# Kernel tuning notes

Measured on AMD Instinct MI355X. Metric: run time of the kernel, lower is better.

Reference implementation:

```python
import jax, jax.numpy as jnp
import numpy as np

D_MODEL = 1024
D_FF = 4096
NUM_EXPERTS = 8
TOP_K = 2
SEQ = 1024
BATCH = 2


def setup_inputs() -> dict:
    key = jax.random.key(0)
    ks = jax.random.split(key, 7)
    s = 0.02
    x = jax.random.normal(ks[0], (SEQ, BATCH, D_MODEL), dtype=jnp.float32)
    gate_w = jax.random.normal(ks[1], (D_MODEL, NUM_EXPERTS), dtype=jnp.float32) * s
    gate_b = jnp.zeros((NUM_EXPERTS,), dtype=jnp.float32)
    W1 = jax.random.normal(ks[2], (NUM_EXPERTS, D_MODEL, D_FF), dtype=jnp.float32) * s
    b1 = jnp.zeros((NUM_EXPERTS, D_FF), dtype=jnp.float32)
    W2 = jax.random.normal(ks[3], (NUM_EXPERTS, D_FF, D_MODEL), dtype=jnp.float32) * s
    b2 = jnp.zeros((NUM_EXPERTS, D_MODEL), dtype=jnp.float32)
    return {"x": x, "gate_w": gate_w, "gate_b": gate_b,
            "W1": W1, "b1": b1, "W2": W2, "b2": b2}


def reference(x, gate_w, gate_b, W1, b1, W2, b2):
    S, B, D = x.shape
    x_flat = x.reshape(-1, D)                       # [T, D], T = S*B
    scores = x_flat @ gate_w + gate_b               # [T, E]
    topk_vals, topk_idx = jax.lax.top_k(scores, TOP_K)   # [T, K]
    topk_probs = jax.nn.softmax(topk_vals, axis=-1)      # [T, K]
    # combine weight per (token, expert): sum of probs over slots routed to e
    one_hot = jax.nn.one_hot(topk_idx, NUM_EXPERTS, dtype=x.dtype)  # [T, K, E]
    combine = jnp.einsum('tk,tke->te', topk_probs, one_hot)         # [T, E]
    # dense per-expert FFN (tokens with combine weight 0 contribute nothing,
    # matching the masked gather/scatter in the torch loop)
    h = jax.nn.relu(jnp.einsum('td,edf->etf', x_flat, W1) + b1[:, None, :])  # [E, T, F]
    y = jnp.einsum('etf,efd->etd', h, W2) + b2[:, None, :]                    # [E, T, D]
    out = jnp.einsum('te,etd->td', combine, y)       # [T, D]
    return out.reshape(S, B, D)
```

## Files before the change

### kernel.cpp

```cpp
#include <hip/hip_runtime.h>
#include <stdint.h>

#define T_TOKENS 2048
#define DM 1024
#define DF 4096
#define NEXP 8
#define NSLOTS (T_TOKENS * 2)

typedef __bf16 bf16x8 __attribute__((ext_vector_type(8)));
typedef float f32x4 __attribute__((ext_vector_type(4)));

__device__ __forceinline__ ushort f2bf(float f) {
    union { float f; uint32_t u; } v; v.f = f;
    uint32_t r = v.u + 0x7FFFu + ((v.u >> 16) & 1u);
    return (ushort)(r >> 16);
}

__device__ __forceinline__ void gload16(const ushort* g, ushort* l) {
    __builtin_amdgcn_global_load_lds(
        (const __attribute__((address_space(1))) uint32_t*)g,
        (__attribute__((address_space(3))) uint32_t*)l,
        16, 0, 0);
}

__global__ void init_cnt(uint32_t* cnt) {
    if (threadIdx.x < NEXP) cnt[threadIdx.x] = 0;
}

__global__ __launch_bounds__(256) void gate_route(
    const float* __restrict__ x, const float* __restrict__ gw,
    const float* __restrict__ gb,
    uint32_t* __restrict__ route, uint32_t* __restrict__ cnt,
    float* __restrict__ prob)
{
    const int w = threadIdx.x >> 6;
    const int lane = threadIdx.x & 63;
    const int t = blockIdx.x * 4 + w;
    float acc[NEXP];
#pragma unroll
    for (int e = 0; e < NEXP; ++e) acc[e] = 0.f;
    const float* xr = x + (size_t)t * DM;
#pragma unroll
    for (int j = 0; j < DM / 64; ++j) {
        const int d = j * 64 + lane;
        const float xv = xr[d];
        const float* g = gw + (size_t)d * NEXP;
#pragma unroll
        for (int e = 0; e < NEXP; ++e) acc[e] += xv * g[e];
    }
#pragma unroll
    for (int e = 0; e < NEXP; ++e) {
#pragma unroll
        for (int off = 32; off > 0; off >>= 1)
            acc[e] += __shfl_xor(acc[e], off);
        acc[e] += gb[e];
    }
    if (lane == 0) {
        int e0 = 0; float v0 = acc[0];
#pragma unroll
        for (int e = 1; e < NEXP; ++e) if (acc[e] > v0) { v0 = acc[e]; e0 = e; }
        int e1 = -1; float v1 = -1e30f;
#pragma unroll
        for (int e = 0; e < NEXP; ++e) if (e != e0 && acc[e] > v1) { v1 = acc[e]; e1 = e; }
        const float ex = expf(v1 - v0);
        const float inv = 1.f / (1.f + ex);
        prob[t * 2 + 0] = inv;
        prob[t * 2 + 1] = ex * inv;
        uint32_t pos = atomicAdd(&cnt[e0], 1u);
        route[e0 * T_TOKENS + pos] = (uint32_t)(t * 2);
        pos = atomicAdd(&cnt[e1], 1u);
        route[e1 * T_TOKENS + pos] = (uint32_t)(t * 2 + 1);
    }
}

__global__ __launch_bounds__(256) void convert_x(const float* __restrict__ x,
                                                 ushort* __restrict__ xb)
{
    const int i = (blockIdx.x * 256 + threadIdx.x) * 4;
    const float4 v = *reinterpret_cast<const float4*>(x + i);
    ushort4 o;
    o.x = f2bf(v.x); o.y = f2bf(v.y); o.z = f2bf(v.z); o.w = f2bf(v.w);
    *reinterpret_cast<ushort4*>(xb + i) = o;
}

template<int K, int N>
__global__ __launch_bounds__(256) void conv_transpose(const float* __restrict__ W,
                                                      ushort* __restrict__ Wb)
{
    const int e  = blockIdx.y;
    const int nt = blockIdx.x % (N / 64);
    const int kt = blockIdx.x / (N / 64);
    const int k0 = kt * 64, n0 = nt * 64;
    __shared__ ushort T[64][80];
    const int t = threadIdx.x;
    const int kr = t >> 4, nc = (t & 15) * 4;
    const float* src = W + ((size_t)e * K + k0 + kr) * N + n0 + nc;
#pragma unroll
    for (int i = 0; i < 4; ++i) {
        const float4 v = *reinterpret_cast<const float4*>(src + (size_t)i * 16 * N);
        T[nc + 0][kr + i * 16] = f2bf(v.x);
        T[nc + 1][kr + i * 16] = f2bf(v.y);
        T[nc + 2][kr + i * 16] = f2bf(v.z);
        T[nc + 3][kr + i * 16] = f2bf(v.w);
    }
    __syncthreads();
    const int r = t >> 2, c0 = t & 3;
    ushort* dst = Wb + ((size_t)e * N + n0 + r) * K + k0;
#pragma unroll
    for (int i = 0; i < 2; ++i) {
        const int c = c0 + i * 4;
        const uint4 v = *reinterpret_cast<const uint4*>(&T[r][c * 8]);
        *reinterpret_cast<uint4*>(dst + c * 8) = v;
    }
}

template<int KD, int ND, bool FIRST, int SPLIT, int NT>
__global__ __launch_bounds__(256, 4) void moe_gemm5(
    const ushort* __restrict__ Abuf,
    const ushort* __restrict__ Wb,
    const float* __restrict__ bias,
    const uint32_t* __restrict__ route,
    const uint32_t* __restrict__ cnt,
    const float* __restrict__ prob,
    ushort* __restrict__ hout,
    float* __restrict__ yout)
{
    const int bx = blockIdx.x;
    const int e  = bx / (16 * NT);
    const int mt = (bx / NT) & 15;
    const int nt = bx % NT;
    const uint32_t cntE = cnt[e];
    const int m0 = mt * 128;
    if ((uint32_t)m0 >= cntE) return;
    const int n0 = nt * 128;
    const int z  = (SPLIT > 1) ? (int)blockIdx.z : 0;
    const int kbeg = z * (KD / SPLIT);
    const int niter = (KD / SPLIT) / 32;

    __shared__ ushort As[2][128 * 32];
    __shared__ ushort Bs[2][128 * 32];
    __shared__ uint32_t s_route[128];

    const int tid = threadIdx.x;
    if (tid < 128) {
        const uint32_t idx = (uint32_t)(m0 + tid);
        s_route[tid] = (idx < cntE) ? route[e * T_TOKENS + idx] : 0xFFFFFFFFu;
    }
    __syncthreads();

    const int w = tid >> 6, l = tid & 63;

    const ushort* asrc[2];
    const ushort* bsrc[2];
#pragma unroll
    for (int i = 0; i < 2; ++i) {
        const int chunk = (w * 2 + i) * 64 + l;
        const int row = chunk >> 2;
        const int c   = chunk & 3;
        const int cs  = c ^ ((row >> 1) & 3);
        const uint32_t s = s_route[row];
        const size_t ar = (s == 0xFFFFFFFFu) ? 0 : (FIRST ? (size_t)(s >> 1) : (size_t)s);
        asrc[i] = Abuf + ar * KD + cs * 8 + kbeg;
        bsrc[i] = Wb + ((size_t)e * ND + n0 + row) * KD + cs * 8 + kbeg;
    }

    f32x4 acc[4][4];
#pragma unroll
    for (int i = 0; i < 4; ++i)
#pragma unroll
        for (int j = 0; j < 4; ++j) acc[i][j] = (f32x4){0.f, 0.f, 0.f, 0.f};

    const int q = l & 15, g = l >> 4;
    const int wm = w >> 1, wn = w & 1;

    int aoff[4], boff[4];
#pragma unroll
    for (int mi = 0; mi < 4; ++mi) {
        int row = wm * 64 + mi * 16 + q;
        aoff[mi] = row * 64 + (g ^ ((row >> 1) & 3)) * 16;
        row = wn * 64 + mi * 16 + q;
        boff[mi] = row * 64 + (g ^ ((row >> 1) & 3)) * 16;
    }

    ushort* const abase0 = &As[0][0];
    ushort* const bbase0 = &Bs[0][0];

#pragma unroll
    for (int i = 0; i < 2; ++i) gload16(asrc[i], abase0 + (w * 2 + i) * 512);
#pragma unroll
    for (int i = 0; i < 2; ++i) gload16(bsrc[i], bbase0 + (w * 2 + i) * 512);

    int cur = 0;
    for (int t = 0; t < niter; ++t) {
        if (t + 1 < niter) {
            ushort* ad = abase0 + (cur ^ 1) * (128 * 32) + (w * 2) * 512;
            ushort* bd = bbase0 + (cur ^ 1) * (128 * 32) + (w * 2) * 512;
            const int k1 = (t + 1) * 32;
#pragma unroll
            for (int i = 0; i < 2; ++i) gload16(asrc[i] + k1, ad + i * 512);
#pragma unroll
            for (int i = 0; i < 2; ++i) gload16(bsrc[i] + k1, bd + i * 512);
            asm volatile("s_waitcnt vmcnt(4)" ::: "memory");
        } else {
            asm volatile("s_waitcnt vmcnt(0)" ::: "memory");
        }
        __builtin_amdgcn_s_barrier();
        __builtin_amdgcn_sched_barrier(0);

        const char* Ab = (const char*)(abase0 + cur * (128 * 32));
        const char* Bb = (const char*)(bbase0 + cur * (128 * 32));
        bf16x8 af[4], bv[4];
#pragma unroll
        for (int mi = 0; mi < 4; ++mi)
            af[mi] = *reinterpret_cast<const bf16x8*>(Ab + aoff[mi]);
#pragma unroll
        for (int ni = 0; ni < 4; ++ni)
            bv[ni] = *reinterpret_cast<const bf16x8*>(Bb + boff[ni]);
        __builtin_amdgcn_s_setprio(1);
#pragma unroll
        for (int mi = 0; mi < 4; ++mi)
#pragma unroll
            for (int ni = 0; ni < 4; ++ni)
                acc[mi][ni] = __builtin_amdgcn_mfma_f32_16x16x32_bf16(
                    af[mi], bv[ni], acc[mi][ni], 0, 0, 0);
        __builtin_amdgcn_s_setprio(0);
        __builtin_amdgcn_s_barrier();
        cur ^= 1;
    }

    const float* brow = bias + (size_t)e * ND;
#pragma unroll
    for (int mi = 0; mi < 4; ++mi) {
#pragma unroll
        for (int ni = 0; ni < 4; ++ni) {
            const int gcol = n0 + wn * 64 + ni * 16 + q;
            const float bv = (SPLIT == 1 || z == 0) ? brow[gcol] : 0.f;
#pragma unroll
            for (int j = 0; j < 4; ++j) {
                const int row = wm * 64 + mi * 16 + g * 4 + j;
                if ((uint32_t)(m0 + row) < cntE) {
                    const uint32_t s = s_route[row];
                    float v = acc[mi][ni][j] + bv;
                    if (FIRST) {
                        v = fmaxf(v, 0.f);
                        hout[(size_t)s * ND + gcol] = f2bf(v);
                    } else {
                        yout[((size_t)z * NSLOTS + s) * ND + gcol] = v * prob[s];
                    }
                }
            }
        }
    }
}

__global__ __launch_bounds__(256) void combine4(const float* __restrict__ yc,
                                                float* __restrict__ out)
{
    const int gid = blockIdx.x * 256 + threadIdx.x;
    const int t = gid >> 8;
    const int dq = gid & 255;
    const float4* Y = reinterpret_cast<const float4*>(yc);
    float4 o = {0.f, 0.f, 0.f, 0.f};
#pragma unroll
    for (int zz = 0; zz < 4; ++zz) {
#pragma unroll
        for (int k = 0; k < 2; ++k) {
            const float4 v = Y[((size_t)zz * NSLOTS + 2 * t + k) * 256 + dq];
            o.x += v.x; o.y += v.y; o.z += v.z; o.w += v.w;
        }
    }
    reinterpret_cast<float4*>(out)[gid] = o;
}

template<int KD, int ND, bool FIRST>
__global__ __launch_bounds__(256) void moe_gemm_v1(
    const ushort* __restrict__ Abuf, const float* __restrict__ W,
    const float* __restrict__ bias, const uint32_t* __restrict__ route,
    const uint32_t* __restrict__ cnt, const float* __restrict__ prob,
    ushort* __restrict__ hout, float* __restrict__ yout)
{
    const int e = blockIdx.x >> 4;
    const int mt = blockIdx.x & 15;
    const uint32_t cntE = cnt[e];
    const int m0 = mt * 128;
    if ((uint32_t)m0 >= cntE) return;
    const int n0 = blockIdx.y * 128;
    const int tid = threadIdx.x;
    __shared__ ushort Asm[128][40];
    __shared__ ushort Bsm[128][40];
    __shared__ uint32_t s_route[128];
    if (tid < 128) {
        const uint32_t idx = (uint32_t)(m0 + tid);
        s_route[tid] = (idx < cntE) ? route[e * T_TOKENS + idx] : 0xFFFFFFFFu;
    }
    __syncthreads();
    const int ar = tid >> 1, ah = tid & 1;
    const uint32_t s_a = s_route[ar];
    size_t arow = 0;
    if (s_a != 0xFFFFFFFFu) arow = FIRST ? (size_t)(s_a >> 1) : (size_t)s_a;
    const ushort* asrc = Abuf + arow * KD + ah * 16;
    const int c4 = tid & 31, kq = tid >> 5;
    const float* wbase = W + (size_t)e * KD * ND + (size_t)n0 + (size_t)c4 * 4;
    f32x4 acc[4][4];
#pragma unroll
    for (int i = 0; i < 4; ++i)
#pragma unroll
        for (int j = 0; j < 4; ++j) acc[i][j] = (f32x4){0.f, 0.f, 0.f, 0.f};
    const int lane = tid & 63, wv = tid >> 6;
    const int wm = wv >> 1, wn = wv & 1;
    const int q = lane & 15, g = lane >> 4;
    for (int k0 = 0; k0 < KD; k0 += 32) {
        {
            const uint4* src = reinterpret_cast<const uint4*>(asrc + k0);
            const uint4 v0 = src[0];
            const uint4 v1 = src[1];
            *reinterpret_cast<uint4*>(&Asm[ar][ah * 16]) = v0;
            *reinterpret_cast<uint4*>(&Asm[ar][ah * 16 + 8]) = v1;
        }
        {
            ushort vals[4][4];
#pragma unroll
            for (int r = 0; r < 4; ++r) {
                const float4 v = *reinterpret_cast<const float4*>(
                    wbase + (size_t)(k0 + kq * 4 + r) * ND);
                vals[r][0] = f2bf(v.x); vals[r][1] = f2bf(v.y);
                vals[r][2] = f2bf(v.z); vals[r][3] = f2bf(v.w);
            }
#pragma unroll
            for (int c = 0; c < 4; ++c) {
                const ushort4 o = { vals[0][c], vals[1][c], vals[2][c], vals[3][c] };
                *reinterpret_cast<ushort4*>(&Bsm[c4 * 4 + c][kq * 4]) = o;
            }
        }
        __syncthreads();
        bf16x8 af[4], bfr[4];
#pragma unroll
        for (int mi = 0; mi < 4; ++mi)
            af[mi] = *reinterpret_cast<const bf16x8*>(&Asm[wm * 64 + mi * 16 + q][g * 8]);
#pragma unroll
        for (int ni = 0; ni < 4; ++ni)
            bfr[ni] = *reinterpret_cast<const bf16x8*>(&Bsm[wn * 64 + ni * 16 + q][g * 8]);
#pragma unroll
        for (int mi = 0; mi < 4; ++mi)
#pragma unroll
            for (int ni = 0; ni < 4; ++ni)
                acc[mi][ni] = __builtin_amdgcn_mfma_f32_16x16x32_bf16(
                    af[mi], bfr[ni], acc[mi][ni], 0, 0, 0);
        __syncthreads();
    }
#pragma unroll
    for (int mi = 0; mi < 4; ++mi) {
#pragma unroll
        for (int ni = 0; ni < 4; ++ni) {
            const int gcol = n0 + wn * 64 + ni * 16 + q;
#pragma unroll
            for (int j = 0; j < 4; ++j) {
                const int row = wm * 64 + mi * 16 + g * 4 + j;
                if ((uint32_t)(m0 + row) < cntE) {
                    const uint32_t s = s_route[row];
                    float v = acc[mi][ni][j] + bias[e * ND + gcol];
                    if (FIRST) {
                        v = fmaxf(v, 0.f);
                        hout[(size_t)s * ND + gcol] = f2bf(v);
                    } else {
                        yout[(size_t)s * ND + gcol] = v * prob[s];
                    }
                }
            }
        }
    }
}

__global__ __launch_bounds__(256) void combine1(const float* __restrict__ yc,
                                                float* __restrict__ out)
{
    const int gid = blockIdx.x * 256 + threadIdx.x;
    const int t = gid >> 8;
    const int dq = gid & 255;
    const float4 va = reinterpret_cast<const float4*>(yc)[(size_t)(2 * t) * 256 + dq];
    const float4 vb = reinterpret_cast<const float4*>(yc)[(size_t)(2 * t + 1) * 256 + dq];
    const float4 o = { va.x + vb.x, va.y + vb.y, va.z + vb.z, va.w + vb.w };
    reinterpret_cast<float4*>(out)[gid] = o;
}

extern "C" void kernel_launch(void* const* d_in, const int* in_sizes, int n_in,
                              void* d_out, int out_size, void* d_ws, size_t ws_size,
                              hipStream_t stream)
{
    const float* x  = (const float*)d_in[0];
    const float* gw = (const float*)d_in[1];
    const float* gb = (const float*)d_in[2];
    const float* W1 = (const float*)d_in[3];
    const float* b1 = (const float*)d_in[4];
    const float* W2 = (const float*)d_in[5];
    const float* b2 = (const float*)d_in[6];
    float* out = (float*)d_out;
    char* ws = (char*)d_ws;

    const size_t OFF_XB    = 0;
    const size_t OFF_H     = 4194304;
    const size_t OFF_ROUTE = 37748736;
    const size_t OFF_CNT   = 37814272;
    const size_t OFF_PROB  = 37814336;
    const size_t OFF_W1B   = 38797312;
    const size_t OFF_W2B   = 105906176;
    const size_t OFF_YC    = OFF_W1B;
    const size_t NEED      = 173015040ull;

    if (ws_size >= NEED) {
        ushort*   xb    = (ushort*)(ws + OFF_XB);
        ushort*   h     = (ushort*)(ws + OFF_H);
        float*    yc    = (float*)(ws + OFF_YC);
        uint32_t* route = (uint32_t*)(ws + OFF_ROUTE);
        uint32_t* cnt   = (uint32_t*)(ws + OFF_CNT);
        float*    prob  = (float*)(ws + OFF_PROB);
        ushort*   w1b   = (ushort*)(ws + OFF_W1B);
        ushort*   w2b   = (ushort*)(ws + OFF_W2B);

        hipLaunchKernelGGL(init_cnt, dim3(1), dim3(64), 0, stream, cnt);
        hipLaunchKernelGGL(gate_route, dim3(T_TOKENS / 4), dim3(256), 0, stream,
                           x, gw, gb, route, cnt, prob);
        hipLaunchKernelGGL(convert_x, dim3(T_TOKENS * DM / 1024), dim3(256), 0, stream, x, xb);
        hipLaunchKernelGGL((conv_transpose<DM, DF>), dim3((DM / 64) * (DF / 64), NEXP),
                           dim3(256), 0, stream, W1, w1b);
        hipLaunchKernelGGL((conv_transpose<DF, DM>), dim3((DF / 64) * (DM / 64), NEXP),
                           dim3(256), 0, stream, W2, w2b);
        hipLaunchKernelGGL((moe_gemm5<DM, DF, true, 1, 32>),
                           dim3(NEXP * 16 * 32, 1, 1), dim3(256), 0, stream,
                           xb, w1b, b1, route, cnt, prob, h, (float*)nullptr);
        hipLaunchKernelGGL((moe_gemm5<DF, DM, false, 4, 8>),
                           dim3(NEXP * 16 * 8, 1, 4), dim3(256), 0, stream,
                           h, w2b, b2, route, cnt, prob, (ushort*)nullptr, yc);
        hipLaunchKernelGGL(combine4, dim3(T_TOKENS * DM / 1024), dim3(256), 0, stream, yc, out);
    } else {
        const size_t F_XB = 0, F_H = 4194304, F_YC = 37748736;
        const size_t F_ROUTE = 54525952, F_CNT = 54591488, F_PROB = 54591552;
        ushort*   xb    = (ushort*)(ws + F_XB);
        ushort*   h     = (ushort*)(ws + F_H);
        float*    yc    = (float*)(ws + F_YC);
        uint32_t* route = (uint32_t*)(ws + F_ROUTE);
        uint32_t* cnt   = (uint32_t*)(ws + F_CNT);
        float*    prob  = (float*)(ws + F_PROB);

        hipLaunchKernelGGL(init_cnt, dim3(1), dim3(64), 0, stream, cnt);
        hipLaunchKernelGGL(gate_route, dim3(T_TOKENS / 4), dim3(256), 0, stream,
                           x, gw, gb, route, cnt, prob);
        hipLaunchKernelGGL(convert_x, dim3(T_TOKENS * DM / 1024), dim3(256), 0, stream, x, xb);
        hipLaunchKernelGGL((moe_gemm_v1<DM, DF, true>), dim3(NEXP * 16, DF / 128),
                           dim3(256), 0, stream, xb, W1, b1, route, cnt, prob,
                           h, (float*)nullptr);
        hipLaunchKernelGGL((moe_gemm_v1<DF, DM, false>), dim3(NEXP * 16, DM / 128),
                           dim3(256), 0, stream, h, W2, b2, route, cnt, prob,
                           (ushort*)nullptr, yc);
        hipLaunchKernelGGL(combine1, dim3(T_TOKENS * DM / 1024), dim3(256), 0, stream, yc, out);
    }
}
```

Baseline: 315.7 us.

## Store hidden activations expert-contiguous and fold gate probability into first GEMM

The first GEMM now writes the hidden activations into rows grouped contiguously by expert, using a prefix-sum offset table, and scales them by the routing probability there. The second GEMM then reads its A operand as contiguous rows with no route indirection. Bias and probability handling for the second GEMM move into the combine kernel, which locates each token's two slot rows through a new packed expert/position array. The W2 conversion is also reordered after the first GEMM. This removes gathered reads and the route lookup from the larger GEMM, at the cost of an extra tiny launch and scattered reads in combine.

Result: faster. 305.5 us (-3.2%).

```diff
diff --git a/kernel.cpp b/kernel.cpp
--- a/kernel.cpp
+++ b/kernel.cpp
@@ -6,6 +6,7 @@
 #define DF 4096
 #define NEXP 8
 #define NSLOTS (T_TOKENS * 2)
+#define HROWS (NSLOTS + 128)
 
 typedef __bf16 bf16x8 __attribute__((ext_vector_type(8)));
 typedef float f32x4 __attribute__((ext_vector_type(4)));
@@ -31,7 +32,7 @@
     const float* __restrict__ x, const float* __restrict__ gw,
     const float* __restrict__ gb,
     uint32_t* __restrict__ route, uint32_t* __restrict__ cnt,
-    float* __restrict__ prob)
+    float* __restrict__ prob, uint32_t* __restrict__ epk)
 {
     const int w = threadIdx.x >> 6;
     const int lane = threadIdx.x & 63;
@@ -68,8 +69,21 @@
         prob[t * 2 + 1] = ex * inv;
         uint32_t pos = atomicAdd(&cnt[e0], 1u);
         route[e0 * T_TOKENS + pos] = (uint32_t)(t * 2);
+        epk[t * 2] = ((uint32_t)e0 << 16) | pos;
         pos = atomicAdd(&cnt[e1], 1u);
         route[e1 * T_TOKENS + pos] = (uint32_t)(t * 2 + 1);
+        epk[t * 2 + 1] = ((uint32_t)e1 << 16) | pos;
+    }
+}
+
+__global__ void prefix_offs(const uint32_t* __restrict__ cnt,
+                            uint32_t* __restrict__ offs)
+{
+    if (threadIdx.x == 0) {
+        uint32_t a = 0;
+#pragma unroll
+        for (int e = 0; e < NEXP; ++e) { offs[e] = a; a += cnt[e]; }
+        offs[NEXP] = a;
     }
 }
 
@@ -115,12 +129,13 @@
 }
 
 template<int KD, int ND, bool FIRST, int SPLIT, int NT>
-__global__ __launch_bounds__(256, 4) void moe_gemm5(
+__global__ __launch_bounds__(256, 4) void moe_gemm6(
     const ushort* __restrict__ Abuf,
     const ushort* __restrict__ Wb,
     const float* __restrict__ bias,
     const uint32_t* __restrict__ route,
     const uint32_t* __restrict__ cnt,
+    const uint32_t* __restrict__ offs,
     const float* __restrict__ prob,
     ushort* __restrict__ hout,
     float* __restrict__ yout)
@@ -132,6 +147,7 @@
     const uint32_t cntE = cnt[e];
     const int m0 = mt * 128;
     if ((uint32_t)m0 >= cntE) return;
+    const uint32_t hb = offs[e];
     const int n0 = nt * 128;
     const int z  = (SPLIT > 1) ? (int)blockIdx.z : 0;
     const int kbeg = z * (KD / SPLIT);
@@ -140,13 +156,18 @@
     __shared__ ushort As[2][128 * 32];
     __shared__ ushort Bs[2][128 * 32];
     __shared__ uint32_t s_route[128];
+    __shared__ float s_p[128];
 
     const int tid = threadIdx.x;
-    if (tid < 128) {
-        const uint32_t idx = (uint32_t)(m0 + tid);
-        s_route[tid] = (idx < cntE) ? route[e * T_TOKENS + idx] : 0xFFFFFFFFu;
-    }
-    __syncthreads();
+    if (FIRST) {
+        if (tid < 128) {
+            const uint32_t idx = (uint32_t)(m0 + tid);
+            const uint32_t s = (idx < cntE) ? route[e * T_TOKENS + idx] : 0u;
+            s_route[tid] = s;
+            s_p[tid] = prob[s];
+        }
+        __syncthreads();
+    }
 
     const int w = tid >> 6, l = tid & 63;
 
@@ -158,9 +179,10 @@
         const int row = chunk >> 2;
         const int c   = chunk & 3;
         const int cs  = c ^ ((row >> 1) & 3);
-        const uint32_t s = s_route[row];
-        const size_t ar = (s == 0xFFFFFFFFu) ? 0 : (FIRST ? (size_t)(s >> 1) : (size_t)s);
-        asrc[i] = Abuf + ar * KD + cs * 8 + kbeg;
+        size_t arow;
+        if (FIRST) arow = (size_t)(s_route[row] >> 1);
+        else       arow = (size_t)(hb + m0 + row);
+        asrc[i] = Abuf + arow * KD + cs * 8 + kbeg;
         bsrc[i] = Wb + ((size_t)e * ND + n0 + row) * KD + cs * 8 + kbeg;
     }
 
@@ -228,24 +250,22 @@
         cur ^= 1;
     }
 
-    const float* brow = bias + (size_t)e * ND;
 #pragma unroll
     for (int mi = 0; mi < 4; ++mi) {
 #pragma unroll
         for (int ni = 0; ni < 4; ++ni) {
             const int gcol = n0 + wn * 64 + ni * 16 + q;
-            const float bv = (SPLIT == 1 || z == 0) ? brow[gcol] : 0.f;
 #pragma unroll
             for (int j = 0; j < 4; ++j) {
                 const int row = wm * 64 + mi * 16 + g * 4 + j;
                 if ((uint32_t)(m0 + row) < cntE) {
-                    const uint32_t s = s_route[row];
-                    float v = acc[mi][ni][j] + bv;
+                    const size_t grow = (size_t)(hb + m0 + row);
                     if (FIRST) {
-                        v = fmaxf(v, 0.f);
-                        hout[(size_t)s * ND + gcol] = f2bf(v);
+                        float v = acc[mi][ni][j] + bias[e * ND + gcol];
+                        v = fmaxf(v, 0.f) * s_p[row];
+                        hout[grow * ND + gcol] = f2bf(v);
                     } else {
-                        yout[((size_t)z * NSLOTS + s) * ND + gcol] = v * prob[s];
+                        yout[((size_t)z * NSLOTS + grow) * ND + gcol] = acc[mi][ni][j];
                     }
                 }
             }
@@ -253,21 +273,29 @@
     }
 }
 
-__global__ __launch_bounds__(256) void combine4(const float* __restrict__ yc,
-                                                float* __restrict__ out)
+__global__ __launch_bounds__(256) void combine5(
+    const float* __restrict__ yc, const uint32_t* __restrict__ epk,
+    const uint32_t* __restrict__ offs, const float* __restrict__ prob,
+    const float* __restrict__ b2, float* __restrict__ out)
 {
     const int gid = blockIdx.x * 256 + threadIdx.x;
     const int t = gid >> 8;
     const int dq = gid & 255;
+    const uint32_t p0 = epk[2 * t], p1 = epk[2 * t + 1];
+    const uint32_t e0 = p0 >> 16, e1 = p1 >> 16;
+    const uint32_t r0 = offs[e0] + (p0 & 0xFFFFu);
+    const uint32_t r1 = offs[e1] + (p1 & 0xFFFFu);
+    const float w0 = prob[2 * t], w1 = prob[2 * t + 1];
+    const float4 bb0 = reinterpret_cast<const float4*>(b2 + (size_t)e0 * DM)[dq];
+    const float4 bb1 = reinterpret_cast<const float4*>(b2 + (size_t)e1 * DM)[dq];
+    float4 o = { w0 * bb0.x + w1 * bb1.x, w0 * bb0.y + w1 * bb1.y,
+                 w0 * bb0.z + w1 * bb1.z, w0 * bb0.w + w1 * bb1.w };
     const float4* Y = reinterpret_cast<const float4*>(yc);
-    float4 o = {0.f, 0.f, 0.f, 0.f};
 #pragma unroll
     for (int zz = 0; zz < 4; ++zz) {
-#pragma unroll
-        for (int k = 0; k < 2; ++k) {
-            const float4 v = Y[((size_t)zz * NSLOTS + 2 * t + k) * 256 + dq];
-            o.x += v.x; o.y += v.y; o.z += v.z; o.w += v.w;
-        }
+        const float4 a = Y[((size_t)zz * NSLOTS + r0) * 256 + dq];
+        const float4 b = Y[((size_t)zz * NSLOTS + r1) * 256 + dq];
+        o.x += a.x + b.x; o.y += a.y + b.y; o.z += a.z + b.z; o.w += a.w + b.w;
     }
     reinterpret_cast<float4*>(out)[gid] = o;
 }
@@ -399,13 +427,15 @@
 
     const size_t OFF_XB    = 0;
     const size_t OFF_H     = 4194304;
-    const size_t OFF_ROUTE = 37748736;
-    const size_t OFF_CNT   = 37814272;
-    const size_t OFF_PROB  = 37814336;
-    const size_t OFF_W1B   = 38797312;
-    const size_t OFF_W2B   = 105906176;
+    const size_t OFF_ROUTE = 38797312;
+    const size_t OFF_CNT   = 38862848;
+    const size_t OFF_OFFS  = 38862912;
+    const size_t OFF_PROB  = 38862976;
+    const size_t OFF_EPK   = 38879360;
+    const size_t OFF_W1B   = 41943040;
+    const size_t OFF_W2B   = 109051904;
     const size_t OFF_YC    = OFF_W1B;
-    const size_t NEED      = 173015040ull;
+    const size_t NEED      = 176160768ull;
 
     if (ws_size >= NEED) {
         ushort*   xb    = (ushort*)(ws + OFF_XB);
@@ -413,25 +443,30 @@
         float*    yc    = (float*)(ws + OFF_YC);
         uint32_t* route = (uint32_t*)(ws + OFF_ROUTE);
         uint32_t* cnt   = (uint32_t*)(ws + OFF_CNT);
+        uint32_t* offs  = (uint32_t*)(ws + OFF_OFFS);
         float*    prob  = (float*)(ws + OFF_PROB);
+        uint32_t* epk   = (uint32_t*)(ws + OFF_EPK);
         ushort*   w1b   = (ushort*)(ws + OFF_W1B);
         ushort*   w2b   = (ushort*)(ws + OFF_W2B);
 
         hipLaunchKernelGGL(init_cnt, dim3(1), dim3(64), 0, stream, cnt);
         hipLaunchKernelGGL(gate_route, dim3(T_TOKENS / 4), dim3(256), 0, stream,
-                           x, gw, gb, route, cnt, prob);
+                           x, gw, gb, route, cnt, prob, epk);
+        hipLaunchKernelGGL(prefix_offs, dim3(1), dim3(64), 0, stream, cnt, offs);
         hipLaunchKernelGGL(convert_x, dim3(T_TOKENS * DM / 1024), dim3(256), 0, stream, x, xb);
         hipLaunchKernelGGL((conv_transpose<DM, DF>), dim3((DM / 64) * (DF / 64), NEXP),
                            dim3(256), 0, stream, W1, w1b);
+        hipLaunchKernelGGL((moe_gemm6<DM, DF, true, 1, 32>),
+                           dim3(NEXP * 16 * 32, 1, 1), dim3(256), 0, stream,
+                           xb, w1b, b1, route, cnt, offs, prob, h, (float*)nullptr);
         hipLaunchKernelGGL((conv_transpose<DF, DM>), dim3((DF / 64) * (DM / 64), NEXP),
                            dim3(256), 0, stream, W2, w2b);
-        hipLaunchKernelGGL((moe_gemm5<DM, DF, true, 1, 32>),
-                           dim3(NEXP * 16 * 32, 1, 1), dim3(256), 0, stream,
-                           xb, w1b, b1, route, cnt, prob, h, (float*)nullptr);
-        hipLaunchKernelGGL((moe_gemm5<DF, DM, false, 4, 8>),
+        hipLaunchKernelGGL((moe_gemm6<DF, DM, false, 4, 8>),
                            dim3(NEXP * 16 * 8, 1, 4), dim3(256), 0, stream,
-                           h, w2b, b2, route, cnt, prob, (ushort*)nullptr, yc);
-        hipLaunchKernelGGL(combine4, dim3(T_TOKENS * DM / 1024), dim3(256), 0, stream, yc, out);
+                           h, w2b, (const float*)nullptr, route, cnt, offs,
+                           (const float*)nullptr, (ushort*)nullptr, yc);
+        hipLaunchKernelGGL(combine5, dim3(T_TOKENS * DM / 1024), dim3(256), 0, stream,
+                           yc, epk, offs, prob, b2, out);
     } else {
         const size_t F_XB = 0, F_H = 4194304, F_YC = 37748736;
         const size_t F_ROUTE = 54525952, F_CNT = 54591488, F_PROB = 54591552;
@@ -441,10 +476,11 @@
         uint32_t* route = (uint32_t*)(ws + F_ROUTE);
         uint32_t* cnt   = (uint32_t*)(ws + F_CNT);
         float*    prob  = (float*)(ws + F_PROB);
+        uint32_t* epk   = (uint32_t*)(ws + F_PROB + 16384);
 
         hipLaunchKernelGGL(init_cnt, dim3(1), dim3(64), 0, stream, cnt);
         hipLaunchKernelGGL(gate_route, dim3(T_TOKENS / 4), dim3(256), 0, stream,
-                           x, gw, gb, route, cnt, prob);
+                           x, gw, gb, route, cnt, prob, epk);
         hipLaunchKernelGGL(convert_x, dim3(T_TOKENS * DM / 1024), dim3(256), 0, stream, x, xb);
         hipLaunchKernelGGL((moe_gemm_v1<DM, DF, true>), dim3(NEXP * 16, DF / 128),
                            dim3(256), 0, stream, xb, W1, b1, route, cnt, prob,
```
